# Performance work log

Measured on AMD Instinct MI355X. Metric: run time of the kernel, lower is better.

Reference implementation:

```python
import jax, jax.numpy as jnp
import numpy as np

N = 12288      # num_nodes
D = 128        # seg_emb
NUM_GRAPHS = 48
NUM_CLS = 27   # classes 24,25,26 are excluded by the module


def setup_inputs() -> dict:
    key = jax.random.key(0)
    k1, k2, k3, k4 = jax.random.split(key, 4)
    z1 = jax.random.normal(k1, (N, D), dtype=jnp.float32)
    z2 = jax.random.normal(k2, (N, D), dtype=jnp.float32)
    cls_label = jax.random.randint(k3, (N,), 0, NUM_CLS, dtype=jnp.int32)
    batch = jnp.sort(jax.random.randint(k4, (N,), 0, NUM_GRAPHS, dtype=jnp.int32))
    return {"z1": z1, "z2": z2, "cls_label": cls_label, "batch": batch}


def reference(z1, z2, cls_label, batch):
    # Pairwise validity mask: same graph AND same class AND class not in {24,25,26}.
    # This reproduces the nested gather->matmul->scatter loops: each (graph, class)
    # block of z1 @ z2.T is kept, everything else stays zero. Single-node classes
    # (skipped in the original) only contribute a diagonal entry, which is zeroed.
    same_graph = batch[:, None] == batch[None, :]            # [N, N]
    same_cls = cls_label[:, None] == cls_label[None, :]      # [N, N]
    excluded = (cls_label >= 24) & (cls_label <= 26)         # [N]
    mask = same_graph & same_cls & ~excluded[:, None]

    scores = jnp.matmul(z1, z2.T)                            # [N, N] inner products
    out = jnp.where(mask, scores, jnp.float32(0.0))
    n = out.shape[0]
    idx = jnp.arange(n)
    out = out.at[idx, idx].set(0.0)                          # zero the diagonal
    return out
```

## Files before the change

kernel.cpp:

```cpp
#include <hip/hip_runtime.h>

#define NN 12288
#define DD 128

typedef float v4f __attribute__((ext_vector_type(4)));

__global__ __launch_bounds__(256, 2) void segdec_fused(
    const float* __restrict__ z1, const float* __restrict__ z2,
    const int* __restrict__ cls, const int* __restrict__ batch,
    float* __restrict__ out)
{
    const int bid = (int)blockIdx.x;
    const int i   = (bid & 7) * (NN >> 3) + (bid >> 3);
    const int tid = threadIdx.x;

    v4f* __restrict__ orow = reinterpret_cast<v4f*>(out + (size_t)i * NN);
    const v4f zero4 = {0.f, 0.f, 0.f, 0.f};

    #pragma unroll
    for (int k = 0; k < 12; ++k)
        __builtin_nontemporal_store(zero4, &orow[tid + (k << 8)]);

    const int cls_i = cls[i];
    if (cls_i >= 24) return;

    const int batch_i = batch[i];
    int lo, hi;
    {
        int l = 0, r = NN;
        while (l < r) { const int m = (l + r) >> 1; if (batch[m] <  batch_i) l = m + 1; else r = m; }
        lo = l;
        r = NN;
        while (l < r) { const int m = (l + r) >> 1; if (batch[m] <= batch_i) l = m + 1; else r = m; }
        hi = l;
    }

    unsigned band_mask = 0u;
    #pragma unroll
    for (int k = 0; k < 12; ++k) {
        const int c0 = (tid + (k << 8)) << 2;
        if (c0 < hi && c0 + 4 > lo) band_mask |= (1u << k);
    }

    if (band_mask) {
        asm volatile("s_waitcnt vmcnt(0)" ::: "memory");

        const v4f* __restrict__ za = reinterpret_cast<const v4f*>(z1 + (size_t)i * DD);
        while (band_mask) {
            const int k = __builtin_ctz(band_mask);
            band_mask &= band_mask - 1;
            const int f4 = tid + (k << 8);
            const int c0 = f4 << 2;
            float vv[4] = {0.f, 0.f, 0.f, 0.f};
            #pragma unroll
            for (int u = 0; u < 4; ++u) {
                const int j = c0 + u;
                if (j >= lo && j < hi && j != i && cls[j] == cls_i) {
                    const v4f* __restrict__ zb =
                        reinterpret_cast<const v4f*>(z2 + (size_t)j * DD);
                    float s = 0.f;
                    #pragma unroll
                    for (int d = 0; d < DD / 4; ++d) {
                        const v4f a = za[d];
                        const v4f b = zb[d];
                        s = fmaf(a.x, b.x, s);
                        s = fmaf(a.y, b.y, s);
                        s = fmaf(a.z, b.z, s);
                        s = fmaf(a.w, b.w, s);
                    }
                    vv[u] = s;
                }
            }
            const v4f v = {vv[0], vv[1], vv[2], vv[3]};
            __builtin_nontemporal_store(v, &orow[f4]);
        }
    }
}

extern "C" void kernel_launch(void* const* d_in, const int* in_sizes, int n_in,
                              void* d_out, int out_size, void* d_ws, size_t ws_size,
                              hipStream_t stream) {
    const float* z1    = (const float*)d_in[0];
    const float* z2    = (const float*)d_in[1];
    const int*   cls   = (const int*)d_in[2];
    const int*   batch = (const int*)d_in[3];
    float*       out   = (float*)d_out;

    segdec_fused<<<NN, 256, 0, stream>>>(z1, z2, cls, batch, out);
}
```

Before: 646.6 us.

## Precompute graph segment starts and split zero-fill from in-band compute blocks

A small pre-kernel builds graph start offsets so the main kernel no longer runs per-row binary searches. The main kernel interleaves two block types. One writes zeros only outside each row's graph band, four rows per block. The other computes dot products only over the band columns with scalar stores, so no element is written twice. The change also drops nontemporal stores and adds a second kernel launch, and band writes become scalar rather than vector stores.

```diff
diff --git a/kernel.cpp b/kernel.cpp
--- a/kernel.cpp
+++ b/kernel.cpp
@@ -2,77 +2,82 @@
 
 #define NN 12288
 #define DD 128
+#define NG 48
 
 typedef float v4f __attribute__((ext_vector_type(4)));
 
-__global__ __launch_bounds__(256, 2) void segdec_fused(
+__global__ __launch_bounds__(256) void build_starts(
+    const int* __restrict__ batch, int* __restrict__ start)
+{
+    for (int j = threadIdx.x; j <= NN; j += 256) {
+        if (j == NN) {
+            const int b = batch[NN - 1];
+            for (int g = b + 1; g <= NG; ++g) start[g] = NN;
+        } else {
+            const int b = batch[j];
+            const int bprev = (j == 0) ? -1 : batch[j - 1];
+            for (int g = bprev + 1; g <= b; ++g) start[g] = j;
+        }
+    }
+}
+
+__global__ __launch_bounds__(256) void segdec_main(
     const float* __restrict__ z1, const float* __restrict__ z2,
     const int* __restrict__ cls, const int* __restrict__ batch,
-    float* __restrict__ out)
+    const int* __restrict__ start, float* __restrict__ out)
 {
     const int bid = (int)blockIdx.x;
-    const int i   = (bid & 7) * (NN >> 3) + (bid >> 3);
-    const int tid = threadIdx.x;
-
-    v4f* __restrict__ orow = reinterpret_cast<v4f*>(out + (size_t)i * NN);
+    const int tid = (int)threadIdx.x;
     const v4f zero4 = {0.f, 0.f, 0.f, 0.f};
 
-    #pragma unroll
-    for (int k = 0; k < 12; ++k)
-        __builtin_nontemporal_store(zero4, &orow[tid + (k << 8)]);
-
-    const int cls_i = cls[i];
-    if (cls_i >= 24) return;
-
-    const int batch_i = batch[i];
-    int lo, hi;
-    {
-        int l = 0, r = NN;
-        while (l < r) { const int m = (l + r) >> 1; if (batch[m] <  batch_i) l = m + 1; else r = m; }
-        lo = l;
-        r = NN;
-        while (l < r) { const int m = (l + r) >> 1; if (batch[m] <= batch_i) l = m + 1; else r = m; }
-        hi = l;
-    }
-
-    unsigned band_mask = 0u;
-    #pragma unroll
-    for (int k = 0; k < 12; ++k) {
-        const int c0 = (tid + (k << 8)) << 2;
-        if (c0 < hi && c0 + 4 > lo) band_mask |= (1u << k);
-    }
-
-    if (band_mask) {
-        asm volatile("s_waitcnt vmcnt(0)" ::: "memory");
+    if (bid % 5 == 0) {
+        const int z = bid / 5;
+        #pragma unroll
+        for (int r = 0; r < 4; ++r) {
+            const int i = (z << 2) + r;
+            const int b = batch[i];
+            const int lo = start[b];
+            const int hi = start[b + 1];
+            const int c0 = lo >> 2;
+            const int c1 = (hi - 1) >> 2;
+            v4f* __restrict__ orow = reinterpret_cast<v4f*>(out + (size_t)i * NN);
+            #pragma unroll
+            for (int k = 0; k < 12; ++k) {
+                const int c = tid + (k << 8);
+                if (c < c0 || c > c1) orow[c] = zero4;
+            }
+        }
+    } else {
+        const int i = bid - bid / 5 - 1;
+        const int cls_i = cls[i];
+        const int b = batch[i];
+        const int lo = start[b];
+        const int hi = start[b + 1];
+        const int c0 = lo >> 2;
+        const int c1 = (hi - 1) >> 2;
+        const int jbase = c0 << 2;
+        const int ncols = ((c1 + 1) << 2) - jbase;
 
         const v4f* __restrict__ za = reinterpret_cast<const v4f*>(z1 + (size_t)i * DD);
-        while (band_mask) {
-            const int k = __builtin_ctz(band_mask);
-            band_mask &= band_mask - 1;
-            const int f4 = tid + (k << 8);
-            const int c0 = f4 << 2;
-            float vv[4] = {0.f, 0.f, 0.f, 0.f};
-            #pragma unroll
-            for (int u = 0; u < 4; ++u) {
-                const int j = c0 + u;
-                if (j >= lo && j < hi && j != i && cls[j] == cls_i) {
-                    const v4f* __restrict__ zb =
-                        reinterpret_cast<const v4f*>(z2 + (size_t)j * DD);
-                    float s = 0.f;
-                    #pragma unroll
-                    for (int d = 0; d < DD / 4; ++d) {
-                        const v4f a = za[d];
-                        const v4f b = zb[d];
-                        s = fmaf(a.x, b.x, s);
-                        s = fmaf(a.y, b.y, s);
-                        s = fmaf(a.z, b.z, s);
-                        s = fmaf(a.w, b.w, s);
-                    }
-                    vv[u] = s;
+        float* __restrict__ orow = out + (size_t)i * NN;
+
+        for (int t = tid; t < ncols; t += 256) {
+            const int j = jbase + t;
+            float s = 0.f;
+            if (cls_i < 24 && j >= lo && j < hi && j != i && cls[j] == cls_i) {
+                const v4f* __restrict__ zb =
+                    reinterpret_cast<const v4f*>(z2 + (size_t)j * DD);
+                #pragma unroll
+                for (int d = 0; d < DD / 4; ++d) {
+                    const v4f a = za[d];
+                    const v4f b4 = zb[d];
+                    s = fmaf(a.x, b4.x, s);
+                    s = fmaf(a.y, b4.y, s);
+                    s = fmaf(a.z, b4.z, s);
+                    s = fmaf(a.w, b4.w, s);
                 }
             }
-            const v4f v = {vv[0], vv[1], vv[2], vv[3]};
-            __builtin_nontemporal_store(v, &orow[f4]);
+            orow[j] = s;
         }
     }
 }
@@ -85,6 +90,8 @@
     const int*   cls   = (const int*)d_in[2];
     const int*   batch = (const int*)d_in[3];
     float*       out   = (float*)d_out;
+    int*         start = (int*)d_ws;
 
-    segdec_fused<<<NN, 256, 0, stream>>>(z1, z2, cls, batch, out);
+    build_starts<<<1, 256, 0, stream>>>(batch, start);
+    segdec_main<<<NN + NN / 4, 256, 0, stream>>>(z1, z2, cls, batch, start, out);
 }
```

New measurement: 648.9 us. Within noise of the previous version (+0.4%).
